# Kernel optimization log

Hardware: AMD Instinct MI355X
Metric: run time of the kernel (lower is better)

Reference implementation:

```python
import jax, jax.numpy as jnp
import numpy as np

S = 4096      # keystrokes
H = 32        # hidden_dim / d_model
NH = 8        # nhead
HD = H // NH  # head dim = 4
FF = 2048     # torch TransformerEncoderLayer default dim_feedforward
NL = 6        # num_layers
EPS = 1e-5


def setup_inputs() -> dict:
    key = jax.random.key(0)
    ks = jax.random.split(key, 20)
    sc = 0.02
    ts = jnp.sort(jax.random.uniform(ks[0], (S,), minval=0.0, maxval=2.49e7))
    feats = jax.random.normal(ks[1], (S, 2), dtype=jnp.float32)
    data = jnp.concatenate([ts[:, None], feats], axis=1)  # [S, 3]
    return {
        "data": data,
        "lin_w": jax.random.normal(ks[2], (H, 2)) * sc,
        "lin_b": jnp.zeros((H,)),
        "qkv_w": jax.random.normal(ks[3], (NL, 3 * H, H)) * sc,
        "qkv_b": jnp.zeros((NL, 3 * H)),
        "out_w": jax.random.normal(ks[4], (NL, H, H)) * sc,
        "out_b": jnp.zeros((NL, H)),
        "ln1_g": jnp.ones((NL, H)),
        "ln1_b": jnp.zeros((NL, H)),
        "ff1_w": jax.random.normal(ks[5], (NL, FF, H)) * sc,
        "ff1_b": jnp.zeros((NL, FF)),
        "ff2_w": jax.random.normal(ks[6], (NL, H, FF)) * sc,
        "ff2_b": jnp.zeros((NL, H)),
        "ln2_g": jnp.ones((NL, H)),
        "ln2_b": jnp.zeros((NL, H)),
        "cls_w": jax.random.normal(ks[7], (1, H)) * sc,
        "cls_b": jnp.zeros((1,)),
    }


def _ln(x, g, b):
    m = x.mean(-1, keepdims=True)
    v = ((x - m) ** 2).mean(-1, keepdims=True)
    return (x - m) / jnp.sqrt(v + EPS) * g + b


def reference(data, lin_w, lin_b, qkv_w, qkv_b, out_w, out_b,
              ln1_g, ln1_b, ff1_w, ff1_b, ff2_w, ff2_b,
              ln2_g, ln2_b, cls_w, cls_b):
    # per-keystroke Linear+ReLU, vectorized over the sequence
    x = jax.nn.relu(data[:, 1:] @ lin_w.T + lin_b)            # [S, H]
    # sinusoidal time encoding at index timestamp//100
    ts_idx = (data[:, 0] / 100.0).astype(jnp.int32)            # [S]
    div = jnp.exp(jnp.arange(0, H, 2, dtype=jnp.float32) * (-np.log(10000.0) / H))
    ang = ts_idx[:, None].astype(jnp.float32) * div            # [S, H/2]
    pe = jnp.stack([jnp.sin(ang), jnp.cos(ang)], axis=-1).reshape(S, H)
    x = x + pe
    # prepend CLS token of -1.0 -> seq len S+1
    x = jnp.concatenate([jnp.full((1, H), -1.0, dtype=x.dtype), x], axis=0)
    L = S + 1
    for i in range(NL):  # post-LN encoder layers (torch defaults, eval/no-dropout)
        qkv = x @ qkv_w[i].T + qkv_b[i]                        # [L, 3H]
        q, k, v = jnp.split(qkv, 3, axis=-1)
        q = q.reshape(L, NH, HD)
        k = k.reshape(L, NH, HD)
        v = v.reshape(L, NH, HD)
        scores = jnp.einsum('qhd,khd->hqk', q, k) / np.sqrt(HD)
        attn = jax.nn.softmax(scores, axis=-1)                 # [NH, L, L]
        o = jnp.einsum('hqk,khd->qhd', attn, v).reshape(L, H)
        o = o @ out_w[i].T + out_b[i]
        x = _ln(x + o, ln1_g[i], ln1_b[i])
        f = jax.nn.relu(x @ ff1_w[i].T + ff1_b[i]) @ ff2_w[i].T + ff2_b[i]
        x = _ln(x + f, ln2_g[i], ln2_b[i])
    cls_out = x[0]                                             # [H]
    return jax.nn.sigmoid(cls_out @ cls_w.T + cls_b)           # [1]
```

## Files before the change

### kernel.cpp

```cpp
#include <hip/hip_runtime.h>
#include <hip/hip_bf16.h>
#include <math.h>

#define SEQ 4096
#define LL  4097
#define HDIM 32
#define FFD 2048
#define NLAYER 6
#define EPSLN 1e-5f
#define NCHUNK 8
#define KPAD 4128
#define QROWS 4352
#define XROWS 4160
#define RT 64
#define FS 128
#define NSEG 8

#if __has_builtin(__builtin_amdgcn_exp2f)
#define EXP2 __builtin_amdgcn_exp2f
#else
#define EXP2 exp2f
#endif

#define QSCALE 0.7213475204444817f

typedef short bf16x8 __attribute__((ext_vector_type(8)));
typedef short bf16x4 __attribute__((ext_vector_type(4)));
typedef float f32x4 __attribute__((ext_vector_type(4)));

__device__ __forceinline__ unsigned short f2b(float f) {
  unsigned int b = __float_as_uint(f);
  b += 0x7FFFu + ((b >> 16) & 1u);
  return (unsigned short)(b >> 16);
}

__device__ __forceinline__ unsigned int pk_bf16(float a, float b) {
  __hip_bfloat162 h = __float22bfloat162_rn(make_float2(a, b));
  return *(unsigned int*)&h;
}

__device__ __forceinline__ f32x4 mfma_qk(bf16x4 a, bf16x4 b, f32x4 c) {
#if __has_builtin(__builtin_amdgcn_mfma_f32_16x16x16bf16_1k)
  return __builtin_amdgcn_mfma_f32_16x16x16bf16_1k(a, b, c, 0, 0, 0);
#else
  bf16x8 a8 = {a[0], a[1], a[2], a[3], 0, 0, 0, 0};
  bf16x8 b8 = {b[0], b[1], b[2], b[3], 0, 0, 0, 0};
  return __builtin_amdgcn_mfma_f32_16x16x32_bf16(a8, b8, c, 0, 0, 0);
#endif
}


__device__ __forceinline__ void qkv_wave(float y, int row, bool ok, int lane,
    const float* __restrict__ qw, const float* __restrict__ qb,
    unsigned short* __restrict__ Qb, unsigned short* __restrict__ KB4,
    unsigned short* __restrict__ VB5) {
  int ch = lane & 31;
  float xv[32];
#pragma unroll
  for (int k = 0; k < 32; ++k) xv[k] = __shfl(y, (lane & 32) + k, 64);
#pragma unroll
  for (int t3 = 0; t3 < 3; ++t3) {
    int cc = t3 * 32 + ch;
    const float4* wr = (const float4*)(qw + (size_t)cc * 32);
    float acc = qb[cc];
#pragma unroll
    for (int k8 = 0; k8 < 8; ++k8) {
      float4 wv = wr[k8];
      acc = fmaf(xv[4 * k8 + 0], wv.x, acc);
      acc = fmaf(xv[4 * k8 + 1], wv.y, acc);
      acc = fmaf(xv[4 * k8 + 2], wv.z, acc);
      acc = fmaf(xv[4 * k8 + 3], wv.w, acc);
    }
    if (ok) {
      int h = ch >> 2;
      if (t3 == 0) {
        Qb[(size_t)row * 32 + ch] = f2b(QSCALE * acc);
      } else if (t3 == 1) {
        KB4[((size_t)h * KPAD + row) * 4 + (ch & 3)] = f2b(acc);
      } else {
        int w = row & 31;
        int pos = ((w & 15) << 1) | (w >> 4);
        VB5[((size_t)h * 5 + (ch & 3)) * KPAD + (row & ~31) + pos] = f2b(acc);
      }
    }
  }
}

__global__ __launch_bounds__(256) void k_init(const float* __restrict__ data,
    const float* __restrict__ lin_w, const float* __restrict__ lin_b,
    const float* __restrict__ qkv_w, const float* __restrict__ qkv_b,
    const float* __restrict__ ff1_w, const float* __restrict__ ff2_w,
    float* __restrict__ X, unsigned short* __restrict__ Qb,
    unsigned short* __restrict__ KB4, unsigned short* __restrict__ VB5,
    unsigned short* __restrict__ W1B, unsigned short* __restrict__ W2B) {
  int gid = blockIdx.x * 256 + threadIdx.x;
  int gsz = gridDim.x * 256;
  const int NW = NLAYER * FFD * 32;
  for (int i = gid; i < NW; i += gsz) {
    W1B[i] = f2b(ff1_w[i]);
    W2B[i] = f2b(ff2_w[i]);
  }
  for (int i = gid; i < (QROWS - LL) * 32; i += gsz)
    Qb[(size_t)LL * 32 + i] = 0;
  for (int i = gid; i < 8 * (KPAD - LL) * 4; i += gsz) {
    int hh = i / ((KPAD - LL) * 4);
    int rem = i % ((KPAD - LL) * 4);
    KB4[((size_t)hh * KPAD + LL) * 4 + rem] = 0;
  }
  for (int i = gid; i < 8 * 5 * KPAD; i += gsz) {
    int col = i % KPAD;
    int dd = (i / KPAD) % 5;
    if (dd == 4) {
      int key = (col & ~31) + ((col & 1) << 4) + ((col & 31) >> 1);
      VB5[i] = (key <= 4096) ? 0x3F80 : 0;
    } else if (col > 4096) {
      VB5[i] = 0;
    }
  }
  int wave = threadIdx.x >> 6, lane = threadIdx.x & 63;
  int r = lane >> 5, ch = lane & 31;
  unsigned wgid = blockIdx.x * 4 + wave;
  for (unsigned it = wgid; it < 2049; it += gridDim.x * 4) {
    int row = it * 2 + r;
    bool ok = row < LL;
    float val = 0.f;
    if (ok) {
      if (row == 0) {
        val = -1.0f;
      } else {
        int s = row - 1;
        float ts = data[s * 3 + 0];
        float f0 = data[s * 3 + 1];
        float f1 = data[s * 3 + 2];
        float lin = f0 * lin_w[ch * 2 + 0] + f1 * lin_w[ch * 2 + 1] + lin_b[ch];
        lin = fmaxf(lin, 0.0f);
        int tsi = (int)(ts / 100.0f);
        int j = ch >> 1;
        float aj = (float)(2 * j) * (float)(-0.28782313662425575);
        float divj = (float)exp((double)aj);
        float ang = (float)tsi * divj;
        float pe = (ch & 1) ? cosf(ang) : sinf(ang);
        val = lin + pe;
      }
      X[(size_t)row * HDIM + ch] = val;
    }
    qkv_wave(val, row, ok, lane, qkv_w, qkv_b, Qb, KB4, VB5);
  }
}

__global__ __launch_bounds__(256, 4) void k_attn(
    const unsigned short* __restrict__ Qb, const unsigned short* __restrict__ KB4,
    const unsigned short* __restrict__ VB5, float* __restrict__ LP,
    float4* __restrict__ AP4) {
  int tid = threadIdx.x;
  int wave = tid >> 6, lane = tid & 63;
  int l16 = lane & 15, quad = lane >> 4;
  int h = blockIdx.y, c = blockIdx.z;
  int qs = blockIdx.x * 4 + wave;
  if (qs >= 65) return;
  int q0 = qs * 64;
  int kb0 = c * 512;
  int nkb = (c == NCHUNK - 1) ? 17 : 16;

  const unsigned short* KBh = KB4 + (size_t)h * KPAD * 4;
  const unsigned short* VBh = VB5 + (size_t)h * 5 * KPAD;
  const bool kl = (quad == (h & 3));
  const bool vl = (l16 < 5);
  const int qcol0 = (h >> 2) * 16 + quad * 4;

  bf16x4 aq[4];
#pragma unroll
  for (int t = 0; t < 4; ++t)
    aq[t] = *(const bf16x4*)&Qb[(size_t)(q0 + t * 16 + l16) * 32 + qcol0];

  const bf16x4 zb4 = {0, 0, 0, 0};
  const bf16x8 zb8 = {0, 0, 0, 0, 0, 0, 0, 0};
  f32x4 acc0[4], acc1[4];
#pragma unroll
  for (int t = 0; t < 4; ++t) {
    acc0[t] = (f32x4){0.f, 0.f, 0.f, 0.f};
    acc1[t] = (f32x4){0.f, 0.f, 0.f, 0.f};
  }

  auto step = [&](int k0, f32x4* acc) {
    bf16x4 bk0 = kl ? *(const bf16x4*)&KBh[(size_t)(k0 + l16) * 4] : zb4;
    bf16x4 bk1 = kl ? *(const bf16x4*)&KBh[(size_t)(k0 + 16 + l16) * 4] : zb4;
    bf16x8 bv = vl ? *(const bf16x8*)&VBh[(size_t)l16 * KPAD + k0 + quad * 8]
                   : zb8;
    f32x4 z = {0.f, 0.f, 0.f, 0.f};
    unsigned pf[4][4];
#pragma unroll
    for (int t = 0; t < 4; ++t) {
      f32x4 s0 = mfma_qk(bk0, aq[t], z);
      f32x4 s1 = mfma_qk(bk1, aq[t], z);
#pragma unroll
      for (int reg = 0; reg < 4; ++reg)
        pf[t][reg] = pk_bf16(EXP2(s0[reg]), EXP2(s1[reg]));
    }
#pragma unroll
    for (int t = 0; t < 4; ++t) {
      bf16x8 pb = *(const bf16x8*)&pf[t][0];
      acc[t] = __builtin_amdgcn_mfma_f32_16x16x32_bf16(bv, pb, acc[t], 0, 0, 0);
    }
  };

  int kb = 0;
  for (; kb + 2 <= nkb; kb += 2) {
    step(kb0 + kb * 32, acc0);
    step(kb0 + (kb + 1) * 32, acc1);
  }
  if (kb < nkb) step(kb0 + kb * 32, acc0);

#pragma unroll
  for (int t = 0; t < 4; ++t) {
    f32x4 a = acc0[t] + acc1[t];
    int q = q0 + t * 16 + l16;
    if (q < LL) {
      if (quad == 0) {
        AP4[((size_t)c * LL + q) * 8 + h] = make_float4(a[0], a[1], a[2], a[3]);
      } else if (quad == 1) {
        LP[((size_t)c * LL + q) * 8 + h] = a[0];
      }
    }
  }
}

__global__ __launch_bounds__(256) void k_oproj(const float* __restrict__ LP,
    const float* __restrict__ APf, float* __restrict__ x,
    unsigned short* __restrict__ Xb,
    const float* __restrict__ ow, const float* __restrict__ ob,
    const float* __restrict__ g, const float* __restrict__ bln) {
  int tid = threadIdx.x;
  int wave = tid >> 6, lane = tid & 63;
  int r = lane >> 5, ch = lane & 31;
  int row = blockIdx.x * 8 + wave * 2 + r;
  bool ok = row < LL;
  int hh = ch >> 2;
  float L = 0.f, A = 0.f;
  if (ok) {
#pragma unroll
    for (int c = 0; c < NCHUNK; ++c) {
      A += APf[((size_t)c * LL + row) * 32 + ch];
      L += LP[((size_t)c * LL + row) * 8 + hh];
    }
  }
  float os = ok ? A / L : 0.f;
  float acc = 0.f;
  const float4* owr = (const float4*)(ow + (size_t)ch * 32);
#pragma unroll
  for (int k8 = 0; k8 < 8; ++k8) {
    float4 wv = owr[k8];
    acc = fmaf(__shfl(os, (lane & 32) + 4 * k8 + 0, 64), wv.x, acc);
    acc = fmaf(__shfl(os, (lane & 32) + 4 * k8 + 1, 64), wv.y, acc);
    acc = fmaf(__shfl(os, (lane & 32) + 4 * k8 + 2, 64), wv.z, acc);
    acc = fmaf(__shfl(os, (lane & 32) + 4 * k8 + 3, 64), wv.w, acc);
  }
  float val = ok ? (x[(size_t)row * HDIM + ch] + acc + ob[ch]) : 0.f;
  float mean = val;
#pragma unroll
  for (int off = 16; off > 0; off >>= 1) mean += __shfl_xor(mean, off, 32);
  mean *= (1.f / 32.f);
  float d2 = val - mean;
  float var = d2 * d2;
#pragma unroll
  for (int off = 16; off > 0; off >>= 1) var += __shfl_xor(var, off, 32);
  var *= (1.f / 32.f);
  float y = d2 / sqrtf(var + EPSLN) * g[ch] + bln[ch];
  if (ok) {
    x[(size_t)row * HDIM + ch] = y;
    Xb[(size_t)row * HDIM + ch] = f2b(y);
  }
}

__global__ __launch_bounds__(256) void k_ffnA(
    const unsigned short* __restrict__ Xb,
    const unsigned short* __restrict__ w1b, const float* __restrict__ b1,
    const unsigned short* __restrict__ w2b, float* __restrict__ part2) {
  __shared__ unsigned short Fsb[RT * 136];
  int tid = threadIdx.x;
  int r0 = blockIdx.x * RT;
  int wave = tid >> 6, lane = tid & 63;
  int l16 = lane & 15, quad = lane >> 4;
  int m0 = wave * 16;

  bf16x8 a1 = *(const bf16x8*)&Xb[(size_t)(r0 + m0 + l16) * 32 + quad * 8];
  f32x4 acc[2] = {{0.f, 0.f, 0.f, 0.f}, {0.f, 0.f, 0.f, 0.f}};

#pragma unroll
  for (int sg = 0; sg < 2; ++sg) {
    int f0 = (blockIdx.y * 2 + sg) * FS;
    f32x4 c1[8];
#pragma unroll
    for (int t = 0; t < 8; ++t) {
      bf16x8 b =
          *(const bf16x8*)&w1b[(size_t)(f0 + t * 16 + l16) * 32 + quad * 8];
      f32x4 z = {0.f, 0.f, 0.f, 0.f};
      c1[t] = __builtin_amdgcn_mfma_f32_16x16x32_bf16(a1, b, z, 0, 0, 0);
    }
#pragma unroll
    for (int t = 0; t < 8; ++t) {
      float bb = b1[f0 + t * 16 + l16];
#pragma unroll
      for (int reg = 0; reg < 4; ++reg) {
        float v = fmaxf(c1[t][reg] + bb, 0.f);
        int rrow = m0 + quad * 4 + reg;
        Fsb[rrow * 136 + t * 16 + l16] = f2b(v);
      }
    }
#pragma unroll
    for (int kt = 0; kt < 4; ++kt) {
      bf16x8 a2 = *(const bf16x8*)&Fsb[(m0 + l16) * 136 + kt * 32 + quad * 8];
#pragma unroll
      for (int u = 0; u < 2; ++u) {
        bf16x8 b = *(const bf16x8*)&w2b[(size_t)(u * 16 + l16) * FFD + f0 +
                                        kt * 32 + quad * 8];
        acc[u] = __builtin_amdgcn_mfma_f32_16x16x32_bf16(a2, b, acc[u], 0, 0, 0);
      }
    }
  }
#pragma unroll
  for (int u = 0; u < 2; ++u) {
#pragma unroll
    for (int reg = 0; reg < 4; ++reg) {
      int rrow = r0 + m0 + quad * 4 + reg;
      if (rrow < LL)
        part2[((size_t)blockIdx.y * LL + rrow) * HDIM + u * 16 + l16] =
            acc[u][reg];
    }
  }
}

__global__ __launch_bounds__(256) void k_ffnB_qkv(float* __restrict__ x,
    const float* __restrict__ part2, const float* __restrict__ b2,
    const float* __restrict__ g, const float* __restrict__ bln,
    const float* __restrict__ qw, const float* __restrict__ qb,
    unsigned short* __restrict__ Qb, unsigned short* __restrict__ KB4,
    unsigned short* __restrict__ VB5, int do_qkv,
    const float* __restrict__ cw, const float* __restrict__ cb,
    float* __restrict__ out) {
  int tid = threadIdx.x;
  int wave = tid >> 6, lane = tid & 63;
  int r = lane >> 5, ch = lane & 31;
  int row = blockIdx.x * 8 + wave * 2 + r;
  bool ok = row < LL;
  float s = 0.f;
  if (ok) {
#pragma unroll
    for (int q = 0; q < NSEG; ++q)
      s += part2[((size_t)q * LL + row) * HDIM + ch];
  }
  float val = ok ? (x[(size_t)row * HDIM + ch] + s + b2[ch]) : 0.f;
  float mean = val;
#pragma unroll
  for (int off = 16; off > 0; off >>= 1) mean += __shfl_xor(mean, off, 32);
  mean *= (1.f / 32.f);
  float d = val - mean;
  float var = d * d;
#pragma unroll
  for (int off = 16; off > 0; off >>= 1) var += __shfl_xor(var, off, 32);
  var *= (1.f / 32.f);
  float y = d / sqrtf(var + EPSLN) * g[ch] + bln[ch];
  if (ok) x[(size_t)row * HDIM + ch] = y;
  if (!do_qkv) {
    if (blockIdx.x == 0 && wave == 0 && r == 0) {
      float t = y * cw[ch];
#pragma unroll
      for (int off = 16; off > 0; off >>= 1) t += __shfl_xor(t, off, 32);
      if (ch == 0) {
        float z = t + cb[0];
        out[0] = 1.f / (1.f + expf(-z));
      }
    }
    return;
  }
  qkv_wave(y, row, ok, lane, qw, qb, Qb, KB4, VB5);
}

extern "C" void kernel_launch(void* const* d_in, const int* in_sizes, int n_in,
                              void* d_out, int out_size, void* d_ws,
                              size_t ws_size, hipStream_t stream) {
  const float* data  = (const float*)d_in[0];
  const float* lin_w = (const float*)d_in[1];
  const float* lin_b = (const float*)d_in[2];
  const float* qkv_w = (const float*)d_in[3];
  const float* qkv_b = (const float*)d_in[4];
  const float* out_w = (const float*)d_in[5];
  const float* out_b = (const float*)d_in[6];
  const float* ln1_g = (const float*)d_in[7];
  const float* ln1_b = (const float*)d_in[8];
  const float* ff1_w = (const float*)d_in[9];
  const float* ff1_b = (const float*)d_in[10];
  const float* ff2_w = (const float*)d_in[11];
  const float* ff2_b = (const float*)d_in[12];
  const float* ln2_g = (const float*)d_in[13];
  const float* ln2_b = (const float*)d_in[14];
  const float* cls_w = (const float*)d_in[15];
  const float* cls_b = (const float*)d_in[16];

  char* wsb = (char*)d_ws;
  float* X = (float*)wsb;
  unsigned short* Xb  = (unsigned short*)(X + (size_t)LL * 32);
  unsigned short* Qb  = Xb + (size_t)XROWS * 32;
  unsigned short* KB4 = Qb + (size_t)QROWS * 32;
  unsigned short* VB5 = KB4 + (size_t)8 * KPAD * 4;
  unsigned short* W1B = VB5 + (size_t)8 * 5 * KPAD;
  unsigned short* W2B = W1B + (size_t)NLAYER * FFD * 32;
  float4* AP = (float4*)(((size_t)(W2B + (size_t)NLAYER * FFD * 32) + 15) &
                         ~(size_t)15);
  float* LP = (float*)(AP + (size_t)NCHUNK * LL * 8);
  float* PART2 = (float*)AP;

  const int NROWB = (LL + 7) / 8;

  k_init<<<1024, 256, 0, stream>>>(data, lin_w, lin_b, qkv_w, qkv_b,
                                   ff1_w, ff2_w, X, Qb, KB4, VB5, W1B, W2B);
  for (int l = 0; l < NLAYER; ++l) {
    k_attn<<<dim3(17, 8, NCHUNK), 256, 0, stream>>>(Qb, KB4, VB5, LP, AP);
    k_oproj<<<NROWB, 256, 0, stream>>>(
        LP, (const float*)AP, X, Xb, out_w + (size_t)l * 32 * 32,
        out_b + (size_t)l * 32,
        ln1_g + (size_t)l * 32, ln1_b + (size_t)l * 32);
    k_ffnA<<<dim3((LL + RT - 1) / RT, NSEG), 256, 0, stream>>>(
        Xb, W1B + (size_t)l * FFD * 32, ff1_b + (size_t)l * FFD,
        W2B + (size_t)l * FFD * 32, PART2);
    int nl = l + 1;
    int do_qkv = (nl < NLAYER) ? 1 : 0;
    const float* qw = qkv_w + (size_t)(do_qkv ? nl : 0) * 96 * 32;
    const float* qb = qkv_b + (size_t)(do_qkv ? nl : 0) * 96;
    k_ffnB_qkv<<<NROWB, 256, 0, stream>>>(
        X, PART2, ff2_b + (size_t)l * 32,
        ln2_g + (size_t)l * 32, ln2_b + (size_t)l * 32,
        qw, qb, Qb, KB4, VB5, do_qkv, cls_w, cls_b, (float*)d_out);
  }
}
```

Before: 448.6 us.

## Fuse out-projection and FFN epilogue into producers via last-block atomic counters

The attention kernel now runs the out-projection, residual add and LayerNorm inside whichever block finishes last for each query-row tile, using a per-tile atomic counter with release/acquire fences. The FFN-B LayerNorm and next-layer QKV projection are folded into the FFN kernel the same way. This cuts each layer from four launches to two and removes the launch gaps and dependency stalls between them. The cost is that the epilogue for a tile now runs serially in a single block (256 rows per attention tile), which leaves much of the GPU idle during the tail. It also adds atomics and fences, plus counters reset once per call in the init kernel.

New measurement: 1.473 ms. +228.3%, slower.

```diff
diff --git a/kernel.cpp b/kernel.cpp
--- a/kernel.cpp
+++ b/kernel.cpp
@@ -49,6 +49,21 @@
 #endif
 }
 
+__device__ __forceinline__ bool last_block(unsigned* cnt, int contributors,
+                                           int* lastFlag) {
+  __syncthreads();
+  if (threadIdx.x == 0) {
+    __builtin_amdgcn_fence(__ATOMIC_RELEASE, "agent");
+    unsigned old = __hip_atomic_fetch_add(cnt, 1u, __ATOMIC_RELAXED,
+                                          __HIP_MEMORY_SCOPE_AGENT);
+    *lastFlag = (old == (unsigned)(contributors - 1));
+  }
+  __syncthreads();
+  if (!*lastFlag) return false;
+  if (threadIdx.x == 0) __builtin_amdgcn_fence(__ATOMIC_ACQUIRE, "agent");
+  __syncthreads();
+  return true;
+}
 
 __device__ __forceinline__ void qkv_wave(float y, int row, bool ok, int lane,
     const float* __restrict__ qw, const float* __restrict__ qb,
@@ -92,9 +107,11 @@
     const float* __restrict__ ff1_w, const float* __restrict__ ff2_w,
     float* __restrict__ X, unsigned short* __restrict__ Qb,
     unsigned short* __restrict__ KB4, unsigned short* __restrict__ VB5,
-    unsigned short* __restrict__ W1B, unsigned short* __restrict__ W2B) {
+    unsigned short* __restrict__ W1B, unsigned short* __restrict__ W2B,
+    unsigned* __restrict__ cnt) {
   int gid = blockIdx.x * 256 + threadIdx.x;
   int gsz = gridDim.x * 256;
+  if (gid < 1024) cnt[gid] = 0;
   const int NW = NLAYER * FFD * 32;
   for (int i = gid; i < NW; i += gsz) {
     W1B[i] = f2b(ff1_w[i]);
@@ -151,132 +168,145 @@
 __global__ __launch_bounds__(256, 4) void k_attn(
     const unsigned short* __restrict__ Qb, const unsigned short* __restrict__ KB4,
     const unsigned short* __restrict__ VB5, float* __restrict__ LP,
-    float4* __restrict__ AP4) {
+    float* __restrict__ APf,
+    float* __restrict__ X, unsigned short* __restrict__ Xb,
+    const float* __restrict__ ow, const float* __restrict__ ob,
+    const float* __restrict__ g1, const float* __restrict__ b1ln,
+    unsigned* __restrict__ cnt) {
+  __shared__ int lastFlag;
   int tid = threadIdx.x;
   int wave = tid >> 6, lane = tid & 63;
   int l16 = lane & 15, quad = lane >> 4;
   int h = blockIdx.y, c = blockIdx.z;
   int qs = blockIdx.x * 4 + wave;
-  if (qs >= 65) return;
-  int q0 = qs * 64;
-  int kb0 = c * 512;
-  int nkb = (c == NCHUNK - 1) ? 17 : 16;
-
-  const unsigned short* KBh = KB4 + (size_t)h * KPAD * 4;
-  const unsigned short* VBh = VB5 + (size_t)h * 5 * KPAD;
-  const bool kl = (quad == (h & 3));
-  const bool vl = (l16 < 5);
-  const int qcol0 = (h >> 2) * 16 + quad * 4;
-
-  bf16x4 aq[4];
-#pragma unroll
-  for (int t = 0; t < 4; ++t)
-    aq[t] = *(const bf16x4*)&Qb[(size_t)(q0 + t * 16 + l16) * 32 + qcol0];
-
-  const bf16x4 zb4 = {0, 0, 0, 0};
-  const bf16x8 zb8 = {0, 0, 0, 0, 0, 0, 0, 0};
-  f32x4 acc0[4], acc1[4];
-#pragma unroll
-  for (int t = 0; t < 4; ++t) {
-    acc0[t] = (f32x4){0.f, 0.f, 0.f, 0.f};
-    acc1[t] = (f32x4){0.f, 0.f, 0.f, 0.f};
-  }
-
-  auto step = [&](int k0, f32x4* acc) {
-    bf16x4 bk0 = kl ? *(const bf16x4*)&KBh[(size_t)(k0 + l16) * 4] : zb4;
-    bf16x4 bk1 = kl ? *(const bf16x4*)&KBh[(size_t)(k0 + 16 + l16) * 4] : zb4;
-    bf16x8 bv = vl ? *(const bf16x8*)&VBh[(size_t)l16 * KPAD + k0 + quad * 8]
-                   : zb8;
-    f32x4 z = {0.f, 0.f, 0.f, 0.f};
-    unsigned pf[4][4];
+  if (qs < 65) {
+    int q0 = qs * 64;
+    int kb0 = c * 512;
+    int nkb = (c == NCHUNK - 1) ? 17 : 16;
+
+    const unsigned short* KBh = KB4 + (size_t)h * KPAD * 4;
+    const unsigned short* VBh = VB5 + (size_t)h * 5 * KPAD;
+    const bool kl = (quad == (h & 3));
+    const bool vl = (l16 < 5);
+    const int qcol0 = (h >> 2) * 16 + quad * 4;
+
+    bf16x4 aq[4];
+#pragma unroll
+    for (int t = 0; t < 4; ++t)
+      aq[t] = *(const bf16x4*)&Qb[(size_t)(q0 + t * 16 + l16) * 32 + qcol0];
+
+    const bf16x4 zb4 = {0, 0, 0, 0};
+    const bf16x8 zb8 = {0, 0, 0, 0, 0, 0, 0, 0};
+    f32x4 acc0[4], acc1[4];
 #pragma unroll
     for (int t = 0; t < 4; ++t) {
-      f32x4 s0 = mfma_qk(bk0, aq[t], z);
-      f32x4 s1 = mfma_qk(bk1, aq[t], z);
-#pragma unroll
-      for (int reg = 0; reg < 4; ++reg)
-        pf[t][reg] = pk_bf16(EXP2(s0[reg]), EXP2(s1[reg]));
-    }
+      acc0[t] = (f32x4){0.f, 0.f, 0.f, 0.f};
+      acc1[t] = (f32x4){0.f, 0.f, 0.f, 0.f};
+    }
+
+    auto step = [&](int k0, f32x4* acc) {
+      bf16x4 bk0 = kl ? *(const bf16x4*)&KBh[(size_t)(k0 + l16) * 4] : zb4;
+      bf16x4 bk1 = kl ? *(const bf16x4*)&KBh[(size_t)(k0 + 16 + l16) * 4] : zb4;
+      bf16x8 bv = vl ? *(const bf16x8*)&VBh[(size_t)l16 * KPAD + k0 + quad * 8]
+                     : zb8;
+      f32x4 z = {0.f, 0.f, 0.f, 0.f};
+      unsigned pf[4][4];
+#pragma unroll
+      for (int t = 0; t < 4; ++t) {
+        f32x4 s0 = mfma_qk(bk0, aq[t], z);
+        f32x4 s1 = mfma_qk(bk1, aq[t], z);
+#pragma unroll
+        for (int reg = 0; reg < 4; ++reg)
+          pf[t][reg] = pk_bf16(EXP2(s0[reg]), EXP2(s1[reg]));
+      }
+#pragma unroll
+      for (int t = 0; t < 4; ++t) {
+        bf16x8 pb = *(const bf16x8*)&pf[t][0];
+        acc[t] =
+            __builtin_amdgcn_mfma_f32_16x16x32_bf16(bv, pb, acc[t], 0, 0, 0);
+      }
+    };
+
+    int kb = 0;
+    for (; kb + 2 <= nkb; kb += 2) {
+      step(kb0 + kb * 32, acc0);
+      step(kb0 + (kb + 1) * 32, acc1);
+    }
+    if (kb < nkb) step(kb0 + kb * 32, acc0);
+
 #pragma unroll
     for (int t = 0; t < 4; ++t) {
-      bf16x8 pb = *(const bf16x8*)&pf[t][0];
-      acc[t] = __builtin_amdgcn_mfma_f32_16x16x32_bf16(bv, pb, acc[t], 0, 0, 0);
-    }
-  };
-
-  int kb = 0;
-  for (; kb + 2 <= nkb; kb += 2) {
-    step(kb0 + kb * 32, acc0);
-    step(kb0 + (kb + 1) * 32, acc1);
-  }
-  if (kb < nkb) step(kb0 + kb * 32, acc0);
-
-#pragma unroll
-  for (int t = 0; t < 4; ++t) {
-    f32x4 a = acc0[t] + acc1[t];
-    int q = q0 + t * 16 + l16;
-    if (q < LL) {
-      if (quad == 0) {
-        AP4[((size_t)c * LL + q) * 8 + h] = make_float4(a[0], a[1], a[2], a[3]);
-      } else if (quad == 1) {
-        LP[((size_t)c * LL + q) * 8 + h] = a[0];
-      }
-    }
-  }
-}
-
-__global__ __launch_bounds__(256) void k_oproj(const float* __restrict__ LP,
-    const float* __restrict__ APf, float* __restrict__ x,
-    unsigned short* __restrict__ Xb,
-    const float* __restrict__ ow, const float* __restrict__ ob,
-    const float* __restrict__ g, const float* __restrict__ bln) {
-  int tid = threadIdx.x;
-  int wave = tid >> 6, lane = tid & 63;
-  int r = lane >> 5, ch = lane & 31;
-  int row = blockIdx.x * 8 + wave * 2 + r;
-  bool ok = row < LL;
+      f32x4 a = acc0[t] + acc1[t];
+      int q = q0 + t * 16 + l16;
+      if (q < LL) {
+        if (quad == 0) {
+          *(float4*)&APf[(((size_t)c * LL + q) * 8 + h) * 4] =
+              make_float4(a[0], a[1], a[2], a[3]);
+        } else if (quad == 1) {
+          LP[((size_t)c * LL + q) * 8 + h] = a[0];
+        }
+      }
+    }
+  }
+
+  if (!last_block(cnt + blockIdx.x, 8 * NCHUNK, &lastFlag)) return;
+
+  int rr = lane >> 5, ch = lane & 31;
   int hh = ch >> 2;
-  float L = 0.f, A = 0.f;
-  if (ok) {
-#pragma unroll
-    for (int c = 0; c < NCHUNK; ++c) {
-      A += APf[((size_t)c * LL + row) * 32 + ch];
-      L += LP[((size_t)c * LL + row) * 8 + hh];
-    }
-  }
-  float os = ok ? A / L : 0.f;
-  float acc = 0.f;
   const float4* owr = (const float4*)(ow + (size_t)ch * 32);
-#pragma unroll
-  for (int k8 = 0; k8 < 8; ++k8) {
-    float4 wv = owr[k8];
-    acc = fmaf(__shfl(os, (lane & 32) + 4 * k8 + 0, 64), wv.x, acc);
-    acc = fmaf(__shfl(os, (lane & 32) + 4 * k8 + 1, 64), wv.y, acc);
-    acc = fmaf(__shfl(os, (lane & 32) + 4 * k8 + 2, 64), wv.z, acc);
-    acc = fmaf(__shfl(os, (lane & 32) + 4 * k8 + 3, 64), wv.w, acc);
-  }
-  float val = ok ? (x[(size_t)row * HDIM + ch] + acc + ob[ch]) : 0.f;
-  float mean = val;
-#pragma unroll
-  for (int off = 16; off > 0; off >>= 1) mean += __shfl_xor(mean, off, 32);
-  mean *= (1.f / 32.f);
-  float d2 = val - mean;
-  float var = d2 * d2;
-#pragma unroll
-  for (int off = 16; off > 0; off >>= 1) var += __shfl_xor(var, off, 32);
-  var *= (1.f / 32.f);
-  float y = d2 / sqrtf(var + EPSLN) * g[ch] + bln[ch];
-  if (ok) {
-    x[(size_t)row * HDIM + ch] = y;
-    Xb[(size_t)row * HDIM + ch] = f2b(y);
-  }
-}
-
-__global__ __launch_bounds__(256) void k_ffnA(
+#pragma unroll 2
+  for (int p = 0; p < 32; ++p) {
+    int row = blockIdx.x * 256 + p * 8 + wave * 2 + rr;
+    bool ok = row < LL;
+    float L = 0.f, A = 0.f;
+    if (ok) {
+#pragma unroll
+      for (int c2 = 0; c2 < NCHUNK; ++c2) {
+        A += APf[((size_t)c2 * LL + row) * 32 + ch];
+        L += LP[((size_t)c2 * LL + row) * 8 + hh];
+      }
+    }
+    float os = ok ? A / L : 0.f;
+    float acc = 0.f;
+#pragma unroll
+    for (int k8 = 0; k8 < 8; ++k8) {
+      float4 wv = owr[k8];
+      acc = fmaf(__shfl(os, (lane & 32) + 4 * k8 + 0, 64), wv.x, acc);
+      acc = fmaf(__shfl(os, (lane & 32) + 4 * k8 + 1, 64), wv.y, acc);
+      acc = fmaf(__shfl(os, (lane & 32) + 4 * k8 + 2, 64), wv.z, acc);
+      acc = fmaf(__shfl(os, (lane & 32) + 4 * k8 + 3, 64), wv.w, acc);
+    }
+    float val = ok ? (X[(size_t)row * HDIM + ch] + acc + ob[ch]) : 0.f;
+    float mean = val;
+#pragma unroll
+    for (int off = 16; off > 0; off >>= 1) mean += __shfl_xor(mean, off, 32);
+    mean *= (1.f / 32.f);
+    float d2 = val - mean;
+    float var = d2 * d2;
+#pragma unroll
+    for (int off = 16; off > 0; off >>= 1) var += __shfl_xor(var, off, 32);
+    var *= (1.f / 32.f);
+    float y = d2 / sqrtf(var + EPSLN) * g1[ch] + b1ln[ch];
+    if (ok) {
+      X[(size_t)row * HDIM + ch] = y;
+      Xb[(size_t)row * HDIM + ch] = f2b(y);
+    }
+  }
+}
+
+__global__ __launch_bounds__(256) void k_ffn(
     const unsigned short* __restrict__ Xb,
     const unsigned short* __restrict__ w1b, const float* __restrict__ b1,
-    const unsigned short* __restrict__ w2b, float* __restrict__ part2) {
+    const unsigned short* __restrict__ w2b, float* __restrict__ part2,
+    float* __restrict__ X, const float* __restrict__ b2,
+    const float* __restrict__ g2, const float* __restrict__ bln2,
+    const float* __restrict__ qw, const float* __restrict__ qb,
+    unsigned short* __restrict__ Qb, unsigned short* __restrict__ KB4,
+    unsigned short* __restrict__ VB5, int do_qkv,
+    const float* __restrict__ cw, const float* __restrict__ cb,
+    float* __restrict__ out, unsigned* __restrict__ cnt) {
   __shared__ unsigned short Fsb[RT * 136];
+  __shared__ int lastFlag;
   int tid = threadIdx.x;
   int r0 = blockIdx.x * RT;
   int wave = tid >> 6, lane = tid & 63;
@@ -328,52 +358,41 @@
             acc[u][reg];
     }
   }
-}
-
-__global__ __launch_bounds__(256) void k_ffnB_qkv(float* __restrict__ x,
-    const float* __restrict__ part2, const float* __restrict__ b2,
-    const float* __restrict__ g, const float* __restrict__ bln,
-    const float* __restrict__ qw, const float* __restrict__ qb,
-    unsigned short* __restrict__ Qb, unsigned short* __restrict__ KB4,
-    unsigned short* __restrict__ VB5, int do_qkv,
-    const float* __restrict__ cw, const float* __restrict__ cb,
-    float* __restrict__ out) {
-  int tid = threadIdx.x;
-  int wave = tid >> 6, lane = tid & 63;
-  int r = lane >> 5, ch = lane & 31;
-  int row = blockIdx.x * 8 + wave * 2 + r;
-  bool ok = row < LL;
-  float s = 0.f;
-  if (ok) {
-#pragma unroll
-    for (int q = 0; q < NSEG; ++q)
-      s += part2[((size_t)q * LL + row) * HDIM + ch];
-  }
-  float val = ok ? (x[(size_t)row * HDIM + ch] + s + b2[ch]) : 0.f;
-  float mean = val;
-#pragma unroll
-  for (int off = 16; off > 0; off >>= 1) mean += __shfl_xor(mean, off, 32);
-  mean *= (1.f / 32.f);
-  float d = val - mean;
-  float var = d * d;
-#pragma unroll
-  for (int off = 16; off > 0; off >>= 1) var += __shfl_xor(var, off, 32);
-  var *= (1.f / 32.f);
-  float y = d / sqrtf(var + EPSLN) * g[ch] + bln[ch];
-  if (ok) x[(size_t)row * HDIM + ch] = y;
-  if (!do_qkv) {
-    if (blockIdx.x == 0 && wave == 0 && r == 0) {
+
+  if (!last_block(cnt + blockIdx.x, NSEG, &lastFlag)) return;
+
+  int rr = lane >> 5, ch = lane & 31;
+#pragma unroll 2
+  for (int p = 0; p < 8; ++p) {
+    int row = r0 + p * 8 + wave * 2 + rr;
+    bool ok = row < LL;
+    float s = 0.f;
+    if (ok) {
+#pragma unroll
+      for (int q = 0; q < NSEG; ++q)
+        s += part2[((size_t)q * LL + row) * HDIM + ch];
+    }
+    float val = ok ? (X[(size_t)row * HDIM + ch] + s + b2[ch]) : 0.f;
+    float mean = val;
+#pragma unroll
+    for (int off = 16; off > 0; off >>= 1) mean += __shfl_xor(mean, off, 32);
+    mean *= (1.f / 32.f);
+    float d = val - mean;
+    float var = d * d;
+#pragma unroll
+    for (int off = 16; off > 0; off >>= 1) var += __shfl_xor(var, off, 32);
+    var *= (1.f / 32.f);
+    float y = d / sqrtf(var + EPSLN) * g2[ch] + bln2[ch];
+    if (ok) X[(size_t)row * HDIM + ch] = y;
+    if (do_qkv) {
+      qkv_wave(y, row, ok, lane, qw, qb, Qb, KB4, VB5);
+    } else if (blockIdx.x == 0 && p == 0 && wave == 0 && rr == 0) {
       float t = y * cw[ch];
 #pragma unroll
       for (int off = 16; off > 0; off >>= 1) t += __shfl_xor(t, off, 32);
-      if (ch == 0) {
-        float z = t + cb[0];
-        out[0] = 1.f / (1.f + expf(-z));
-      }
-    }
-    return;
-  }
-  qkv_wave(y, row, ok, lane, qw, qb, Qb, KB4, VB5);
+      if (ch == 0) out[0] = 1.f / (1.f + expf(-(t + cb[0])));
+    }
+  }
 }
 
 extern "C" void kernel_launch(void* const* d_in, const int* in_sizes, int n_in,
@@ -398,38 +417,38 @@
   const float* cls_b = (const float*)d_in[16];
 
   char* wsb = (char*)d_ws;
-  float* X = (float*)wsb;
+  unsigned* cnt = (unsigned*)wsb;
+  float* X = (float*)(wsb + 4096);
   unsigned short* Xb  = (unsigned short*)(X + (size_t)LL * 32);
   unsigned short* Qb  = Xb + (size_t)XROWS * 32;
   unsigned short* KB4 = Qb + (size_t)QROWS * 32;
   unsigned short* VB5 = KB4 + (size_t)8 * KPAD * 4;
   unsigned short* W1B = VB5 + (size_t)8 * 5 * KPAD;
   unsigned short* W2B = W1B + (size_t)NLAYER * FFD * 32;
-  float4* AP = (float4*)(((size_t)(W2B + (size_t)NLAYER * FFD * 32) + 15) &
-                         ~(size_t)15);
-  float* LP = (float*)(AP + (size_t)NCHUNK * LL * 8);
-  float* PART2 = (float*)AP;
-
-  const int NROWB = (LL + 7) / 8;
+  float* APf = (float*)(((size_t)(W2B + (size_t)NLAYER * FFD * 32) + 15) &
+                        ~(size_t)15);
+  float* LP = APf + (size_t)NCHUNK * LL * 32;
+  float* PART2 = APf;
 
   k_init<<<1024, 256, 0, stream>>>(data, lin_w, lin_b, qkv_w, qkv_b,
-                                   ff1_w, ff2_w, X, Qb, KB4, VB5, W1B, W2B);
+                                   ff1_w, ff2_w, X, Qb, KB4, VB5, W1B, W2B,
+                                   cnt);
   for (int l = 0; l < NLAYER; ++l) {
-    k_attn<<<dim3(17, 8, NCHUNK), 256, 0, stream>>>(Qb, KB4, VB5, LP, AP);
-    k_oproj<<<NROWB, 256, 0, stream>>>(
-        LP, (const float*)AP, X, Xb, out_w + (size_t)l * 32 * 32,
-        out_b + (size_t)l * 32,
-        ln1_g + (size_t)l * 32, ln1_b + (size_t)l * 32);
-    k_ffnA<<<dim3((LL + RT - 1) / RT, NSEG), 256, 0, stream>>>(
-        Xb, W1B + (size_t)l * FFD * 32, ff1_b + (size_t)l * FFD,
-        W2B + (size_t)l * FFD * 32, PART2);
+    k_attn<<<dim3(17, 8, NCHUNK), 256, 0, stream>>>(
+        Qb, KB4, VB5, LP, APf, X, Xb,
+        out_w + (size_t)l * 32 * 32, out_b + (size_t)l * 32,
+        ln1_g + (size_t)l * 32, ln1_b + (size_t)l * 32,
+        cnt + l * 32);
     int nl = l + 1;
     int do_qkv = (nl < NLAYER) ? 1 : 0;
     const float* qw = qkv_w + (size_t)(do_qkv ? nl : 0) * 96 * 32;
     const float* qb = qkv_b + (size_t)(do_qkv ? nl : 0) * 96;
-    k_ffnB_qkv<<<NROWB, 256, 0, stream>>>(
-        X, PART2, ff2_b + (size_t)l * 32,
+    k_ffn<<<dim3((LL + RT - 1) / RT, NSEG), 256, 0, stream>>>(
+        Xb, W1B + (size_t)l * FFD * 32, ff1_b + (size_t)l * FFD,
+        W2B + (size_t)l * FFD * 32, PART2,
+        X, ff2_b + (size_t)l * 32,
         ln2_g + (size_t)l * 32, ln2_b + (size_t)l * 32,
-        qw, qb, Qb, KB4, VB5, do_qkv, cls_w, cls_b, (float*)d_out);
-  }
-}
+        qw, qb, Qb, KB4, VB5, do_qkv, cls_w, cls_b, (float*)d_out,
+        cnt + 192 + l * 128);
+  }
+}
```
